# Performance work log

Hardware: AMD Instinct MI355X
Metric: run time of the kernel (lower is better)

Reference implementation:

```python
import math
import jax, jax.numpy as jnp
import numpy as np

E = 1024
H = 16
D = E // H  # head_dim = 64
B, T = 4, 2048


def setup_inputs() -> dict:
    key = jax.random.key(0)
    ks = jax.random.split(key, 9)
    s = 1.0 / math.sqrt(E)
    inp = {
        "x": jax.random.normal(ks[0], (B, T, E), dtype=jnp.float32),
        "Wq": jax.random.uniform(ks[1], (E, E), jnp.float32, -s, s),
        "bq": jax.random.uniform(ks[2], (E,), jnp.float32, -s, s),
        "Wk": jax.random.uniform(ks[3], (E, E), jnp.float32, -s, s),
        "bk": jax.random.uniform(ks[4], (E,), jnp.float32, -s, s),
        "Wv": jax.random.uniform(ks[5], (E, E), jnp.float32, -s, s),
        "bv": jax.random.uniform(ks[6], (E,), jnp.float32, -s, s),
        "Wo": jax.random.uniform(ks[7], (E, E), jnp.float32, -s, s),
        "bo": jax.random.uniform(ks[8], (E,), jnp.float32, -s, s),
    }
    return inp


def reference(x, Wq, bq, Wk, bk, Wv, bv, Wo, bo):
    # Linear projections (torch Linear: y = x @ W.T + b)
    q = x @ Wq.T + bq
    k = x @ Wk.T + bk
    v = x @ Wv.T + bv
    # [B, T, E] -> [B, H, T, D]
    def split_heads(t):
        return t.reshape(B, T, H, D).transpose(0, 2, 1, 3)
    q, k, v = split_heads(q), split_heads(k), split_heads(v)
    # scaled dot-product attention; note scale uses head_dim (attention(self.head_dim))
    scores = jnp.einsum("bhqd,bhkd->bhqk", q, k) / math.sqrt(D)
    attn = jax.nn.softmax(scores, axis=-1)
    out = jnp.einsum("bhqk,bhkd->bhqd", attn, v)
    out = out.transpose(0, 2, 1, 3).reshape(B, T, E)
    return out @ Wo.T + bo
```

## Files before the change

kernel.cpp:

```cpp
#include <hip/hip_runtime.h>

typedef short bh8 __attribute__((ext_vector_type(8)));
typedef short bh4 __attribute__((ext_vector_type(4)));
typedef float f4 __attribute__((ext_vector_type(4)));
typedef unsigned int u32;
typedef u32 u32x2 __attribute__((ext_vector_type(2)));
typedef u32 u32x4 __attribute__((ext_vector_type(4)));

#if __has_builtin(__builtin_amdgcn_exp2f)
#define EXP2(x) __builtin_amdgcn_exp2f(x)
#else
#define EXP2(x) exp2f(x)
#endif

__device__ __forceinline__ short f2bf(float f) {
  unsigned u = __float_as_uint(f);
  u += 0x7FFFu + ((u >> 16) & 1u);
  return (short)(u >> 16);
}

__device__ __forceinline__ void async16(const void* g, void* l) {
  __builtin_amdgcn_global_load_lds((const __attribute__((address_space(1))) void*)g,
                                   (__attribute__((address_space(3))) void*)l, 16, 0, 0);
}

__global__ void cvt_all(const float* __restrict__ x, const float* __restrict__ Wq,
                        const float* __restrict__ Wk, const float* __restrict__ Wv,
                        const float* __restrict__ Wo, short* __restrict__ xb,
                        short* __restrict__ wqb) {
  int i = blockIdx.x * blockDim.x + threadIdx.x;
  const float* src;
  short* dst;
  int idx;
  if (i < (1 << 21)) {
    src = x; dst = xb; idx = i;
  } else {
    int j = i - (1 << 21);
    int w = j >> 18;
    idx = j & ((1 << 18) - 1);
    src = w == 0 ? Wq : w == 1 ? Wk : w == 2 ? Wv : Wo;
    dst = wqb + ((size_t)w << 20);
  }
  f4 v = *(const f4*)(src + (size_t)idx * 4);
  bh4 o;
  o[0] = f2bf(v[0]); o[1] = f2bf(v[1]); o[2] = f2bf(v[2]); o[3] = f2bf(v[3]);
  *(bh4*)(dst + (size_t)idx * 4) = o;
}

template <typename OutT, bool BROW>
__device__ __forceinline__ void gemm_body(const short* __restrict__ A, const short* __restrict__ Bw,
                                          const float* __restrict__ bias, OutT* __restrict__ C,
                                          int m0, int n0, int N, int K, float scale,
                                          short* a_lds, short* b_lds) {
  const int t = threadIdx.x;
  const int lane = t & 63, wave = t >> 6, quad = lane >> 4, l15 = lane & 15;
  const int mw = (wave >> 1) * 64, nw = (wave & 1) * 64;

  f4 acc[4][4];
#pragma unroll
  for (int i = 0; i < 4; ++i)
#pragma unroll
    for (int j = 0; j < 4; ++j) acc[i][j] = (f4){0.f, 0.f, 0.f, 0.f};

  for (int k0 = 0; k0 < K; k0 += 64) {
    __syncthreads();
#pragma unroll
    for (int i = 0; i < 4; ++i) {
      int c = i * 256 + t;
      int m = c >> 3;
      int kq = (c & 7) ^ (m & 7);
      async16(A + (size_t)(m0 + m) * K + k0 + kq * 8, (char*)a_lds + c * 16);
    }
#pragma unroll
    for (int i = 0; i < 4; ++i) {
      int c = i * 256 + t;
      int m = c >> 3;
      int kq = (c & 7) ^ (m & 7);
      async16(Bw + (size_t)(n0 + m) * K + k0 + kq * 8, (char*)b_lds + c * 16);
    }
    __syncthreads();

#pragma unroll
    for (int s = 0; s < 2; ++s) {
      bh8 af[4], bfr[4];
#pragma unroll
      for (int ms = 0; ms < 4; ++ms) {
        int m = mw + ms * 16 + l15;
        int pos = m * 8 + ((s * 4 + quad) ^ (m & 7));
        af[ms] = *(const bh8*)(a_lds + pos * 8);
      }
#pragma unroll
      for (int ns = 0; ns < 4; ++ns) {
        int n = nw + ns * 16 + l15;
        int pos = n * 8 + ((s * 4 + quad) ^ (n & 7));
        bfr[ns] = *(const bh8*)(b_lds + pos * 8);
      }
#pragma unroll
      for (int ms = 0; ms < 4; ++ms)
#pragma unroll
        for (int ns = 0; ns < 4; ++ns)
          acc[ms][ns] = __builtin_amdgcn_mfma_f32_16x16x32_bf16(af[ms], bfr[ns], acc[ms][ns], 0, 0, 0);
    }
  }
#pragma unroll
  for (int ns = 0; ns < 4; ++ns) {
    int col = n0 + nw + ns * 16 + l15;
    float bcol = BROW ? 0.f : bias[col & 1023];
#pragma unroll
    for (int ms = 0; ms < 4; ++ms) {
      int row = m0 + mw + ms * 16 + quad * 4;
#pragma unroll
      for (int r = 0; r < 4; ++r) {
        float bv = BROW ? bias[(row + r) & 1023] : bcol;
        float v = (acc[ms][ns][r] + bv) * scale;
        if (sizeof(OutT) == 2)
          ((short*)C)[(size_t)(row + r) * N + col] = f2bf(v);
        else
          ((float*)C)[(size_t)(row + r) * N + col] = v;
      }
    }
  }
}

__global__ void gemm_qkv(const short* __restrict__ xb, const short* __restrict__ W3,
                         const float* __restrict__ bq, const float* __restrict__ bk,
                         const float* __restrict__ bv,
                         short* __restrict__ Qo, short* __restrict__ Ko, short* __restrict__ VTo,
                         float qscale) {
  __shared__ __align__(16) short a_lds[128 * 64];
  __shared__ __align__(16) short b_lds[128 * 64];
  const int linear = blockIdx.y * 24 + blockIdx.x;
  const int xcd = linear & 7;
  const int slot = linear >> 3;
  const int byp = xcd * 8 + slot / 24;
  const int rest = slot % 24;
  const int which = rest >> 3;
  const int nx = rest & 7;
  if (which == 2) {
    const short* Wv = W3 + (size_t)2 * 1024 * 1024;
    gemm_body<short, true>(Wv, xb, bv, VTo, nx * 128, byp * 128,
                           8192, 1024, 1.0f, a_lds, b_lds);
  } else {
    const short* Bw = W3 + (size_t)which * 1024 * 1024;
    const float* bias = which == 0 ? bq : bk;
    short* C = which == 0 ? Qo : Ko;
    float scale = which == 0 ? qscale : 1.0f;
    gemm_body<short, false>(xb, Bw, bias, C, byp * 128, nx * 128,
                            1024, 1024, scale, a_lds, b_lds);
  }
}

__global__ void gemm_bt_f32(const short* __restrict__ A, const short* __restrict__ Bw,
                            const float* __restrict__ bias, float* __restrict__ C) {
  __shared__ __align__(16) short a_lds[128 * 64];
  __shared__ __align__(16) short b_lds[64 * 64];
  const int t = threadIdx.x;
  const int lane = t & 63, wave = t >> 6, quad = lane >> 4, l15 = lane & 15;
  const int mw = (wave >> 1) * 64, nw = (wave & 1) * 32;
  const int linear = blockIdx.y * 16 + blockIdx.x;
  const int xcd = linear & 7;
  const int slot = linear >> 3;
  const int m0 = (xcd * 8 + (slot >> 4)) * 128;
  const int n0 = (slot & 15) * 64;

  f4 acc[4][2];
#pragma unroll
  for (int i = 0; i < 4; ++i)
#pragma unroll
    for (int j = 0; j < 2; ++j) acc[i][j] = (f4){0.f, 0.f, 0.f, 0.f};

  for (int k0 = 0; k0 < 1024; k0 += 64) {
    __syncthreads();
#pragma unroll
    for (int i = 0; i < 4; ++i) {
      int c = i * 256 + t;
      int m = c >> 3;
      int kq = (c & 7) ^ (m & 7);
      async16(A + (size_t)(m0 + m) * 1024 + k0 + kq * 8, (char*)a_lds + c * 16);
    }
#pragma unroll
    for (int i = 0; i < 2; ++i) {
      int c = i * 256 + t;
      int m = c >> 3;
      int kq = (c & 7) ^ (m & 7);
      async16(Bw + (size_t)(n0 + m) * 1024 + k0 + kq * 8, (char*)b_lds + c * 16);
    }
    __syncthreads();

#pragma unroll
    for (int s = 0; s < 2; ++s) {
      bh8 af[4], bfr[2];
#pragma unroll
      for (int ms = 0; ms < 4; ++ms) {
        int m = mw + ms * 16 + l15;
        int pos = m * 8 + ((s * 4 + quad) ^ (m & 7));
        af[ms] = *(const bh8*)(a_lds + pos * 8);
      }
#pragma unroll
      for (int ns = 0; ns < 2; ++ns) {
        int n = nw + ns * 16 + l15;
        int pos = n * 8 + ((s * 4 + quad) ^ (n & 7));
        bfr[ns] = *(const bh8*)(b_lds + pos * 8);
      }
#pragma unroll
      for (int ms = 0; ms < 4; ++ms)
#pragma unroll
        for (int ns = 0; ns < 2; ++ns)
          acc[ms][ns] = __builtin_amdgcn_mfma_f32_16x16x32_bf16(af[ms], bfr[ns], acc[ms][ns], 0, 0, 0);
    }
  }
#pragma unroll
  for (int ns = 0; ns < 2; ++ns) {
    int col = n0 + nw + ns * 16 + l15;
    float bcol = bias[col & 1023];
#pragma unroll
    for (int ms = 0; ms < 4; ++ms) {
      int row = m0 + mw + ms * 16 + quad * 4;
#pragma unroll
      for (int r = 0; r < 4; ++r)
        C[(size_t)(row + r) * 1024 + col] = acc[ms][ns][r] + bcol;
    }
  }
}

__global__ void attn_kernel(const short* __restrict__ Qb, const short* __restrict__ Kb,
                            const short* __restrict__ VTb, short* __restrict__ AO) {
  __shared__ __align__(16) short k_lds[64 * 64];
  __shared__ __align__(16) short vt_lds[64 * 64];
  const int t = threadIdx.x, lane = t & 63, wave = t >> 6, quad = lane >> 4, l15 = lane & 15;
  const int linear = blockIdx.y * 16 + blockIdx.x;
  const int xcd = linear & 7;
  const int slot = linear >> 3;
  const int bh = xcd * 8 + (slot >> 4);
  const int qx = slot & 15;
  const int b = bh >> 4, h = bh & 15;
  const int q0 = qx * 128;
  const size_t baseq = ((size_t)b * 2048) * 1024 + (size_t)h * 64;
  const size_t basev = ((size_t)h * 64) * 8192 + (size_t)b * 2048;

  bh8 qf[2][2];
#pragma unroll
  for (int mi = 0; mi < 2; ++mi)
#pragma unroll
    for (int ks = 0; ks < 2; ++ks)
      qf[mi][ks] = *(const bh8*)(Qb + baseq + (size_t)(q0 + wave * 32 + mi * 16 + l15) * 1024 + ks * 32 + quad * 8);

  f4 O[2][4];
  float l_part[2] = {0.f, 0.f};
#pragma unroll
  for (int mi = 0; mi < 2; ++mi)
#pragma unroll
    for (int di = 0; di < 4; ++di) O[mi][di] = (f4){0.f, 0.f, 0.f, 0.f};

  for (int kt = 0; kt < 2048; kt += 64) {
    __syncthreads();
#pragma unroll
    for (int i = 0; i < 2; ++i) {
      int c = i * 256 + t;
      int kk = c >> 3;
      int dq = (c & 7) ^ (kk & 7);
      async16(Kb + baseq + (size_t)(kt + kk) * 1024 + dq * 8,
              (char*)k_lds + (i * 256 + wave * 64) * 16);
    }
#pragma unroll
    for (int i = 0; i < 2; ++i) {
      int c = i * 256 + t;
      int d = c >> 3;
      int kc = (c & 7) ^ (d & 7);
      async16(VTb + basev + (size_t)d * 8192 + kt + kc * 8,
              (char*)vt_lds + (i * 256 + wave * 64) * 16);
    }
    __syncthreads();

    f4 ST[4][2];
#pragma unroll
    for (int mK = 0; mK < 4; ++mK) {
      int key = mK * 16 + l15;
      bh8 ka0 = *(const bh8*)(k_lds + (key * 8 + (quad ^ (key & 7))) * 8);
      bh8 ka1 = *(const bh8*)(k_lds + (key * 8 + ((quad + 4) ^ (key & 7))) * 8);
#pragma unroll
      for (int mi = 0; mi < 2; ++mi) {
        f4 s = (f4){-16.f, -16.f, -16.f, -16.f};
        s = __builtin_amdgcn_mfma_f32_16x16x32_bf16(ka0, qf[mi][0], s, 0, 0, 0);
        s = __builtin_amdgcn_mfma_f32_16x16x32_bf16(ka1, qf[mi][1], s, 0, 0, 0);
        ST[mK][mi] = s;
      }
    }

    bh8 pa[2][2];
#pragma unroll
    for (int mi = 0; mi < 2; ++mi) {
      float lp = 0.f;
      u32 E[4], F[4];
#pragma unroll
      for (int mK = 0; mK < 4; ++mK) {
        float p0 = EXP2(ST[mK][mi][0]);
        float p1 = EXP2(ST[mK][mi][1]);
        float p2 = EXP2(ST[mK][mi][2]);
        float p3 = EXP2(ST[mK][mi][3]);
        lp += (p0 + p1) + (p2 + p3);
        E[mK] = __builtin_amdgcn_perm(__float_as_uint(p1), __float_as_uint(p0), 0x07060302u);
        F[mK] = __builtin_amdgcn_perm(__float_as_uint(p3), __float_as_uint(p2), 0x07060302u);
      }
      l_part[mi] += lp;
#pragma unroll
      for (int ks = 0; ks < 2; ++ks) {
        u32 e0 = E[ks * 2], e1 = E[ks * 2 + 1];
        u32 f0 = F[ks * 2], f1 = F[ks * 2 + 1];
        asm volatile("v_permlane32_swap_b32 %0, %1" : "+v"(e0), "+v"(e1));
        asm volatile("v_permlane16_swap_b32 %0, %1" : "+v"(e0), "+v"(e1));
        asm volatile("v_permlane32_swap_b32 %0, %1" : "+v"(f0), "+v"(f1));
        asm volatile("v_permlane16_swap_b32 %0, %1" : "+v"(f0), "+v"(f1));
        u32x4 w;
        w[0] = e0; w[1] = f0; w[2] = e1; w[3] = f1;
        pa[mi][ks] = __builtin_bit_cast(bh8, w);
      }
    }

#pragma unroll
    for (int di = 0; di < 4; ++di) {
      int d = di * 16 + l15;
      bh8 vb0 = *(const bh8*)(vt_lds + (d * 8 + (quad ^ (d & 7))) * 8);
      bh8 vb1 = *(const bh8*)(vt_lds + (d * 8 + ((quad + 4) ^ (d & 7))) * 8);
#pragma unroll
      for (int mi = 0; mi < 2; ++mi) {
        f4 o = O[mi][di];
        o = __builtin_amdgcn_mfma_f32_16x16x32_bf16(pa[mi][0], vb0, o, 0, 0, 0);
        o = __builtin_amdgcn_mfma_f32_16x16x32_bf16(pa[mi][1], vb1, o, 0, 0, 0);
        O[mi][di] = o;
      }
    }
  }

#pragma unroll
  for (int mi = 0; mi < 2; ++mi) {
    float l0 = l_part[mi];
    l0 += __shfl_xor(l0, 16);
    l0 += __shfl_xor(l0, 32);
    float rl[4];
#pragma unroll
    for (int r = 0; r < 4; ++r) {
      float lb = __shfl(l0, quad * 4 + r);
      rl[r] = __builtin_amdgcn_rcpf(lb);
    }
#pragma unroll
    for (int di = 0; di < 4; ++di)
#pragma unroll
      for (int r = 0; r < 4; ++r) {
        int row = q0 + wave * 32 + mi * 16 + quad * 4 + r;
        AO[baseq + (size_t)row * 1024 + di * 16 + l15] = f2bf(O[mi][di][r] * rl[r]);
      }
  }
}

extern "C" void kernel_launch(void* const* d_in, const int* in_sizes, int n_in,
                              void* d_out, int out_size, void* d_ws, size_t ws_size,
                              hipStream_t stream) {
  const float* x  = (const float*)d_in[0];
  const float* Wq = (const float*)d_in[1];
  const float* bq = (const float*)d_in[2];
  const float* Wk = (const float*)d_in[3];
  const float* bk = (const float*)d_in[4];
  const float* Wv = (const float*)d_in[5];
  const float* bv = (const float*)d_in[6];
  const float* Wo = (const float*)d_in[7];
  const float* bo = (const float*)d_in[8];
  float* out = (float*)d_out;

  const int M = 8192, E = 1024;
  const size_t NX = (size_t)M * E;
  const size_t NW = (size_t)E * E;

  short* ws  = (short*)d_ws;
  short* xb  = ws;
  short* wqb = xb + NX;
  short* wob = wqb + 3 * NW;
  short* qb  = wob + NW;
  short* kb  = qb + NX;
  short* vt  = kb + NX;
  short* aob = xb;

  cvt_all<<<dim3(12288), 256, 0, stream>>>(x, Wq, Wk, Wv, Wo, xb, wqb);

  const float qscale = 0.18033688011112042f;
  gemm_qkv<<<dim3(24, 64), 256, 0, stream>>>(xb, wqb, bq, bk, bv, qb, kb, vt, qscale);

  attn_kernel<<<dim3(16, 64), 256, 0, stream>>>(qb, kb, vt, aob);

  gemm_bt_f32<<<dim3(16, 64), 256, 0, stream>>>(aob, wob, bo, out);
}
```

Before: 259.8 us.

## Enlarge QKV GEMM tiles to 256x128 with 512-thread blocks

The QKV projection GEMM moves from 128x128 tiles with 256 threads to 256x128 tiles with 512 threads (8 waves), launched as a 1D grid of 768 blocks with a new XCD-aware mapping for the Q/K and V^T parts. Each B tile is now reused across twice as many rows, which cuts global and LDS load traffic per MFMA. In exchange the block uses more LDS (48KB), which may lower occupancy, and the grid has fewer, larger blocks. The templated body is inlined and made runtime-branched on bias orientation.

```diff
diff --git a/kernel.cpp b/kernel.cpp
--- a/kernel.cpp
+++ b/kernel.cpp
@@ -47,36 +47,77 @@
   *(bh4*)(dst + (size_t)idx * 4) = o;
 }
 
-template <typename OutT, bool BROW>
-__device__ __forceinline__ void gemm_body(const short* __restrict__ A, const short* __restrict__ Bw,
-                                          const float* __restrict__ bias, OutT* __restrict__ C,
-                                          int m0, int n0, int N, int K, float scale,
-                                          short* a_lds, short* b_lds) {
+__global__ __launch_bounds__(512) void gemm_qkv(const short* __restrict__ xb,
+                                                const short* __restrict__ W3,
+                                                const float* __restrict__ bq,
+                                                const float* __restrict__ bk,
+                                                const float* __restrict__ bv,
+                                                short* __restrict__ Qo, short* __restrict__ Ko,
+                                                short* __restrict__ VTo, float qscale) {
+  __shared__ __align__(16) short a_lds[256 * 64];
+  __shared__ __align__(16) short b_lds[128 * 64];
   const int t = threadIdx.x;
   const int lane = t & 63, wave = t >> 6, quad = lane >> 4, l15 = lane & 15;
   const int mw = (wave >> 1) * 64, nw = (wave & 1) * 64;
 
+  const int linear = blockIdx.x;
+  const int xcd = linear & 7;
+  const int slot = linear >> 3;
+  const short* A;
+  const short* B;
+  const float* bias;
+  short* C;
+  float scale = 1.0f;
+  int m0, n0, N;
+  bool brow;
+  if (slot < 64) {
+    int byp = xcd * 4 + (slot >> 4);
+    int r = slot & 15;
+    int which = r >> 3;
+    int nx = r & 7;
+    m0 = byp * 256;
+    n0 = nx * 128;
+    A = xb;
+    B = W3 + (size_t)which * 1024 * 1024;
+    bias = which == 0 ? bq : bk;
+    C = which == 0 ? Qo : Ko;
+    scale = which == 0 ? qscale : 1.0f;
+    N = 1024;
+    brow = false;
+  } else {
+    int s2 = slot - 64;
+    int nloc = s2 >> 2, mv = s2 & 3;
+    m0 = mv * 256;
+    n0 = (xcd * 8 + nloc) * 128;
+    A = W3 + (size_t)2 * 1024 * 1024;
+    B = xb;
+    bias = bv;
+    C = VTo;
+    N = 8192;
+    brow = true;
+  }
+
   f4 acc[4][4];
 #pragma unroll
   for (int i = 0; i < 4; ++i)
 #pragma unroll
     for (int j = 0; j < 4; ++j) acc[i][j] = (f4){0.f, 0.f, 0.f, 0.f};
 
-  for (int k0 = 0; k0 < K; k0 += 64) {
+  for (int k0 = 0; k0 < 1024; k0 += 64) {
     __syncthreads();
 #pragma unroll
     for (int i = 0; i < 4; ++i) {
-      int c = i * 256 + t;
+      int c = i * 512 + t;
       int m = c >> 3;
       int kq = (c & 7) ^ (m & 7);
-      async16(A + (size_t)(m0 + m) * K + k0 + kq * 8, (char*)a_lds + c * 16);
-    }
-#pragma unroll
-    for (int i = 0; i < 4; ++i) {
-      int c = i * 256 + t;
+      async16(A + (size_t)(m0 + m) * 1024 + k0 + kq * 8, (char*)a_lds + c * 16);
+    }
+#pragma unroll
+    for (int i = 0; i < 2; ++i) {
+      int c = i * 512 + t;
       int m = c >> 3;
       int kq = (c & 7) ^ (m & 7);
-      async16(Bw + (size_t)(n0 + m) * K + k0 + kq * 8, (char*)b_lds + c * 16);
+      async16(B + (size_t)(n0 + m) * 1024 + k0 + kq * 8, (char*)b_lds + c * 16);
     }
     __syncthreads();
 
@@ -105,48 +146,17 @@
 #pragma unroll
   for (int ns = 0; ns < 4; ++ns) {
     int col = n0 + nw + ns * 16 + l15;
-    float bcol = BROW ? 0.f : bias[col & 1023];
+    float bcol = brow ? 0.f : bias[col & 1023];
 #pragma unroll
     for (int ms = 0; ms < 4; ++ms) {
       int row = m0 + mw + ms * 16 + quad * 4;
 #pragma unroll
       for (int r = 0; r < 4; ++r) {
-        float bv = BROW ? bias[(row + r) & 1023] : bcol;
-        float v = (acc[ms][ns][r] + bv) * scale;
-        if (sizeof(OutT) == 2)
-          ((short*)C)[(size_t)(row + r) * N + col] = f2bf(v);
-        else
-          ((float*)C)[(size_t)(row + r) * N + col] = v;
-      }
-    }
-  }
-}
-
-__global__ void gemm_qkv(const short* __restrict__ xb, const short* __restrict__ W3,
-                         const float* __restrict__ bq, const float* __restrict__ bk,
-                         const float* __restrict__ bv,
-                         short* __restrict__ Qo, short* __restrict__ Ko, short* __restrict__ VTo,
-                         float qscale) {
-  __shared__ __align__(16) short a_lds[128 * 64];
-  __shared__ __align__(16) short b_lds[128 * 64];
-  const int linear = blockIdx.y * 24 + blockIdx.x;
-  const int xcd = linear & 7;
-  const int slot = linear >> 3;
-  const int byp = xcd * 8 + slot / 24;
-  const int rest = slot % 24;
-  const int which = rest >> 3;
-  const int nx = rest & 7;
-  if (which == 2) {
-    const short* Wv = W3 + (size_t)2 * 1024 * 1024;
-    gemm_body<short, true>(Wv, xb, bv, VTo, nx * 128, byp * 128,
-                           8192, 1024, 1.0f, a_lds, b_lds);
-  } else {
-    const short* Bw = W3 + (size_t)which * 1024 * 1024;
-    const float* bias = which == 0 ? bq : bk;
-    short* C = which == 0 ? Qo : Ko;
-    float scale = which == 0 ? qscale : 1.0f;
-    gemm_body<short, false>(xb, Bw, bias, C, byp * 128, nx * 128,
-                            1024, 1024, scale, a_lds, b_lds);
+        float bv_ = brow ? bias[(row + r) & 1023] : bcol;
+        float v = (acc[ms][ns][r] + bv_) * scale;
+        C[(size_t)(row + r) * N + col] = f2bf(v);
+      }
+    }
   }
 }
 
@@ -383,7 +393,7 @@
   cvt_all<<<dim3(12288), 256, 0, stream>>>(x, Wq, Wk, Wv, Wo, xb, wqb);
 
   const float qscale = 0.18033688011112042f;
-  gemm_qkv<<<dim3(24, 64), 256, 0, stream>>>(xb, wqb, bq, bk, bv, qb, kb, vt, qscale);
+  gemm_qkv<<<dim3(768), 512, 0, stream>>>(xb, wqb, bq, bk, bv, qb, kb, vt, qscale);
 
   attn_kernel<<<dim3(16, 64), 256, 0, stream>>>(qb, kb, vt, aob);
 
```

After: 271.7 us. 4.6% more time.
